# Kernel optimization log

Measured on AMD Instinct MI355X. Metric: run time of the kernel, lower is better.

## Reference

```python
import jax, jax.numpy as jnp
import numpy as np

NUM_NODES = 16384
EMBED_DIM = 128
BATCH = 32


def setup_inputs() -> dict:
    key = jax.random.key(0)
    k1, k2, k3 = jax.random.split(key, 3)
    # xavier_uniform for embed_node: bound = sqrt(6/(fan_in+fan_out))
    xb = float(np.sqrt(6.0 / (NUM_NODES + EMBED_DIM)))
    embed_node = jax.random.uniform(k1, (NUM_NODES, EMBED_DIM), minval=-xb, maxval=xb, dtype=jnp.float32)
    # nn.Linear default init: U(-1/sqrt(fan_in), 1/sqrt(fan_in)). These params exist but
    # provably do not affect the output (root node at depth 0 is never updated).
    lb = float(np.sqrt(1.0 / EMBED_DIM))
    W_self = jax.random.uniform(k2, (EMBED_DIM, EMBED_DIM), minval=-lb, maxval=lb, dtype=jnp.float32)
    W_child = jax.random.uniform(k3, (EMBED_DIM, EMBED_DIM), minval=-lb, maxval=lb, dtype=jnp.float32)
    return {"embed_node": embed_node, "W_self": W_self, "W_child": W_child, "batch_size": BATCH}


def reference(embed_node, W_self, W_child, batch_size):
    # Faithful math of TreeBasedSpatialEmbedding.forward:
    # - adj_matrix_path=None -> tree_structures is None -> node_emb = embed_node.
    # - (Even with trees: depth-0 root is skipped in _tree_aggregate, so
    #   root_embedding[root_node] == embed_node[root_node]; identical result.)
    # Then: unsqueeze(0).expand(B,-1,-1) -> [B,N,D]; transpose(1,2) -> [B,D,N]; unsqueeze(-1) -> [B,D,N,1]
    n, d = embed_node.shape
    out = jnp.broadcast_to(embed_node.T[None, :, :], (batch_size, d, n))[..., None]
    return out
```

## Files before the change

kernel.cpp:

```cpp
#include <hip/hip_runtime.h>
#include <hip/hip_bf16.h>


#define NN 16384
#define DD 128
#define NB 32
#define NT 64

typedef float f4_t __attribute__((ext_vector_type(4)));

__global__ __launch_bounds__(256) void tree_embed_kernel(
    const float* __restrict__ E, float* __restrict__ out) {
    __shared__ float lds[DD][NT + 1];

    const int n0 = blockIdx.x * NT;
    const int tid = threadIdx.x;

    {
        const int c = tid & 31;
        const int r = tid >> 5;
        #pragma unroll
        for (int it = 0; it < NT / 8; ++it) {
            const int n = r + it * 8;
            const f4_t v = *reinterpret_cast<const f4_t*>(
                &E[(size_t)(n0 + n) * DD + (c << 2)]);
            lds[(c << 2) + 0][n] = v.x;
            lds[(c << 2) + 1][n] = v.y;
            lds[(c << 2) + 2][n] = v.z;
            lds[(c << 2) + 3][n] = v.w;
        }
    }
    __syncthreads();

    const int j = tid & 15;
    const int row0 = tid >> 4;
    #pragma unroll 8
    for (int it = 0; it < (NB * DD) / 16; ++it) {
        const int row = row0 + it * 16;
        const int d = row & (DD - 1);
        const int b = row >> 7;
        f4_t v;
        v.x = lds[d][(j << 2) + 0];
        v.y = lds[d][(j << 2) + 1];
        v.z = lds[d][(j << 2) + 2];
        v.w = lds[d][(j << 2) + 3];
        const size_t oidx = (((size_t)b * DD + d) * NN) + n0 + (j << 2);
        *reinterpret_cast<f4_t*>(&out[oidx]) = v;
    }
}

extern "C" void kernel_launch(void* const* d_in, const int* in_sizes, int n_in,
                              void* d_out, int out_size, void* d_ws, size_t ws_size,
                              hipStream_t stream) {
    const float* E = (const float*)d_in[0];
    float* out = (float*)d_out;
    hipLaunchKernelGGL(tree_embed_kernel, dim3(NN / NT), dim3(256), 0, stream,
                       E, out);
}
```

Measured before the change: 46.15 us.

## Retile transpose-broadcast into 32x256 tiles with vectorized LDS reads

The kernel now tiles over both the embedding dimension (32) and nodes (256) on a 2D grid instead of full-D by 64-node tiles. Each output row segment is written by a full wavefront covering 1 KB contiguous, and LDS rows are padded by 4 so reads can be single 16-byte vector loads instead of four scalar loads. The cost it targets is short 256-byte store runs and scalar LDS traffic. The grid stays at 256 blocks. Padding by 4 may cause LDS bank conflicts on the transposing writes.

```diff
diff --git a/kernel.cpp b/kernel.cpp
--- a/kernel.cpp
+++ b/kernel.cpp
@@ -5,25 +5,27 @@
 #define NN 16384
 #define DD 128
 #define NB 32
-#define NT 64
+#define DT 32
+#define NT 256
 
 typedef float f4_t __attribute__((ext_vector_type(4)));
 
 __global__ __launch_bounds__(256) void tree_embed_kernel(
     const float* __restrict__ E, float* __restrict__ out) {
-    __shared__ float lds[DD][NT + 1];
+    __shared__ float lds[DT][NT + 4];
 
-    const int n0 = blockIdx.x * NT;
+    const int d0 = blockIdx.x * DT;
+    const int n0 = blockIdx.y * NT;
     const int tid = threadIdx.x;
 
     {
-        const int c = tid & 31;
-        const int r = tid >> 5;
+        const int c = tid & 7;
+        const int r0 = tid >> 3;
         #pragma unroll
-        for (int it = 0; it < NT / 8; ++it) {
-            const int n = r + it * 8;
+        for (int i = 0; i < NT / 32; ++i) {
+            const int n = r0 + (i << 5);
             const f4_t v = *reinterpret_cast<const f4_t*>(
-                &E[(size_t)(n0 + n) * DD + (c << 2)]);
+                &E[(size_t)(n0 + n) * DD + d0 + (c << 2)]);
             lds[(c << 2) + 0][n] = v.x;
             lds[(c << 2) + 1][n] = v.y;
             lds[(c << 2) + 2][n] = v.z;
@@ -32,19 +34,15 @@
     }
     __syncthreads();
 
-    const int j = tid & 15;
-    const int row0 = tid >> 4;
+    const int j = tid & 63;
+    const int w = tid >> 6;
     #pragma unroll 8
-    for (int it = 0; it < (NB * DD) / 16; ++it) {
-        const int row = row0 + it * 16;
-        const int d = row & (DD - 1);
-        const int b = row >> 7;
-        f4_t v;
-        v.x = lds[d][(j << 2) + 0];
-        v.y = lds[d][(j << 2) + 1];
-        v.z = lds[d][(j << 2) + 2];
-        v.w = lds[d][(j << 2) + 3];
-        const size_t oidx = (((size_t)b * DD + d) * NN) + n0 + (j << 2);
+    for (int it = 0; it < (NB * DT) / 4; ++it) {
+        const int r = w + (it << 2);
+        const int d = r & (DT - 1);
+        const int b = r >> 5;
+        const f4_t v = *reinterpret_cast<const f4_t*>(&lds[d][j << 2]);
+        const size_t oidx = ((size_t)b * DD + d0 + d) * NN + n0 + (j << 2);
         *reinterpret_cast<f4_t*>(&out[oidx]) = v;
     }
 }
@@ -54,6 +52,6 @@
                               hipStream_t stream) {
     const float* E = (const float*)d_in[0];
     float* out = (float*)d_out;
-    hipLaunchKernelGGL(tree_embed_kernel, dim3(NN / NT), dim3(256), 0, stream,
-                       E, out);
+    dim3 grid(DD / DT, NN / NT);
+    hipLaunchKernelGGL(tree_embed_kernel, grid, dim3(256), 0, stream, E, out);
 }
```

Measured after the change: 45.94 us. About the same (-0.5%).
